# Optimization experiments

Hardware: AMD Instinct MI355X
Metric: run time of the kernel (lower is better)

Reference implementation:

```python
import jax, jax.numpy as jnp
import numpy as np

N_NODES = 50000
N_EDGES = 800000
NODE_DIM = 128
EDGE_DIM = 64
MSG_DIM = 128
IN_DIM = 2 * NODE_DIM + EDGE_DIM  # 320
LN_EPS = 1e-5


def setup_inputs() -> dict:
    key = jax.random.key(0)
    ks = jax.random.split(key, 12)
    nodes = jax.random.normal(ks[0], (N_NODES, NODE_DIM), dtype=jnp.float32)
    edge_index = jax.random.randint(ks[1], (2, N_EDGES), 0, N_NODES, dtype=jnp.int64)
    edges = jax.random.normal(ks[2], (N_EDGES, EDGE_DIM), dtype=jnp.float32)
    # query projection (kaiming-normal weight, zero bias)
    Wq = jax.random.normal(ks[3], (IN_DIM, MSG_DIM), dtype=jnp.float32) * np.sqrt(2.0 / IN_DIM)
    bq = jnp.zeros((MSG_DIM,), dtype=jnp.float32)
    # logit MLP: Linear(IN_DIM->MSG_DIM) -> ReLU -> LayerNorm -> Linear(MSG_DIM->1) -> ReLU
    W1 = jax.random.normal(ks[4], (IN_DIM, MSG_DIM), dtype=jnp.float32) * np.sqrt(1.0 / IN_DIM)
    b1 = jnp.zeros((MSG_DIM,), dtype=jnp.float32)
    gamma = jnp.ones((MSG_DIM,), dtype=jnp.float32)
    beta = jnp.zeros((MSG_DIM,), dtype=jnp.float32)
    W2 = jax.random.normal(ks[5], (MSG_DIM, 1), dtype=jnp.float32) * np.sqrt(1.0 / MSG_DIM)
    b2 = jnp.zeros((1,), dtype=jnp.float32)
    return {"nodes": nodes, "edge_index": edge_index, "edges": edges,
            "Wq": Wq, "bq": bq, "W1": W1, "b1": b1,
            "gamma": gamma, "beta": beta, "W2": W2, "b2": b2}


def _layernorm(h, gamma, beta):
    mu = jnp.mean(h, axis=-1, keepdims=True)
    var = jnp.mean(jnp.square(h - mu), axis=-1, keepdims=True)
    return (h - mu) / jnp.sqrt(var + LN_EPS) * gamma + beta


def _forward(nodes, edges, Wq, bq, W1, b1, gamma, beta, W2, b2, senders, receivers):
    n_nodes = nodes.shape[0]
    x = jnp.concatenate([nodes[senders], nodes[receivers], edges], axis=-1)  # (E, IN_DIM)
    queries = x @ Wq + bq                                                    # (E, MSG_DIM)
    h = jax.nn.relu(x @ W1 + b1)
    h = _layernorm(h, gamma, beta)
    logits = jax.nn.relu(h @ W2 + b2)[:, 0]                                  # (E,)
    # segment softmax over receivers
    seg_max = jax.ops.segment_max(logits, receivers, num_segments=n_nodes)
    seg_max = jnp.where(jnp.isfinite(seg_max), seg_max, 0.0)
    exp_l = jnp.exp(logits - seg_max[receivers])
    seg_sum = jax.ops.segment_sum(exp_l, receivers, num_segments=n_nodes)
    weights = exp_l / (seg_sum[receivers] + 1e-10)                           # (E,)
    messages = queries * weights[:, None]
    out = jax.ops.segment_sum(messages, receivers, num_segments=n_nodes)    # (N, MSG_DIM)
    return jax.nn.leaky_relu(out, negative_slope=0.01)


def reference(nodes, edge_index, edges, Wq, bq, W1, b1, gamma, beta, W2, b2):
    senders, receivers = edge_index[0], edge_index[1]
    return _forward(nodes, edges, Wq, bq, W1, b1, gamma, beta, W2, b2, senders, receivers)
```

## Files before the change

kernel.cpp:

```cpp
#include <hip/hip_runtime.h>
#include <hip/hip_bf16.h>

#define NN 50000
#define NE 800000
#define D 128
#define ED 64
#define IN_DIM 320
#define MB 64
#define KP 328
#define NT (NE / MB)
#define PGRID 512
#define NB ((NN + 255) / 256)

typedef short short8 __attribute__((ext_vector_type(8)));
typedef float f32x4 __attribute__((ext_vector_type(4)));

__device__ __forceinline__ ushort f2b(float f) {
  __hip_bfloat16 h = __float2bfloat16(f);
  return *reinterpret_cast<ushort*>(&h);
}
__device__ __forceinline__ float b2f(ushort u) {
  return __uint_as_float(((uint)u) << 16);
}
__device__ __forceinline__ ushort4 c4(float4 v) {
  ushort4 u; u.x = f2b(v.x); u.y = f2b(v.y); u.z = f2b(v.z); u.w = f2b(v.w);
  return u;
}

__device__ __forceinline__ void gather_regs(
    ushort4 g[20], const int* __restrict__ senders,
    const int* __restrict__ receivers, const float* __restrict__ nodes,
    const float* __restrict__ efeat, int e0, int tid)
{
  const int e = tid >> 2, p = tid & 3;
  const float* ns = nodes + (size_t)senders[e0 + e] * D;
  const float* nr = nodes + (size_t)receivers[e0 + e] * D;
  const float* ef = efeat + (size_t)(e0 + e) * ED;
#pragma unroll
  for (int i = 0; i < 8; ++i) g[i] = c4(*(const float4*)(ns + (p + 4 * i) * 4));
#pragma unroll
  for (int i = 0; i < 8; ++i) g[8 + i] = c4(*(const float4*)(nr + (p + 4 * i) * 4));
#pragma unroll
  for (int i = 0; i < 4; ++i) g[16 + i] = c4(*(const float4*)(ef + (p + 4 * i) * 4));
}

__device__ __forceinline__ void write_xs(
    ushort xs[MB][KP], const ushort4 g[20], int tid)
{
  const int e = tid >> 2, p = tid & 3;
#pragma unroll
  for (int i = 0; i < 8; ++i)
    *reinterpret_cast<ushort4*>(&xs[e][(p + 4 * i) * 4]) = g[i];
#pragma unroll
  for (int i = 0; i < 8; ++i)
    *reinterpret_cast<ushort4*>(&xs[e][128 + (p + 4 * i) * 4]) = g[8 + i];
#pragma unroll
  for (int i = 0; i < 4; ++i)
    *reinterpret_cast<ushort4*>(&xs[e][256 + (p + 4 * i) * 4]) = g[16 + i];
}

__global__ __launch_bounds__(256) void k_wconv(
    const float* __restrict__ Wq, const float* __restrict__ W1,
    ushort* __restrict__ Wqt, ushort* __restrict__ W1t)
{
  int i = blockIdx.x * 256 + threadIdx.x;
  if (i < D * IN_DIM) {
    int n = i / IN_DIM, k = i - n * IN_DIM;
    Wqt[i] = f2b(Wq[k * D + n]);
    W1t[i] = f2b(W1[k * D + n]);
  }
}

__global__ __launch_bounds__(256, 2) void k_fused(
    const float* __restrict__ nodes,
    const int* __restrict__ senders, const int* __restrict__ receivers,
    const float* __restrict__ efeat,
    const ushort* __restrict__ Wqt, const float* __restrict__ bq,
    const ushort* __restrict__ W1t, const float* __restrict__ b1,
    const float* __restrict__ gamma_, const float* __restrict__ beta_,
    const float* __restrict__ W2, const float* __restrict__ b2,
    ushort* __restrict__ queries, float* __restrict__ logits,
    float* __restrict__ seg_max)
{
  __shared__ ushort xs[MB][KP];
  __shared__ float red[MB][4][3];
  const int tid = threadIdx.x;
  const int w = tid >> 6, l = tid & 63, lr = l & 15, lg = l >> 4;
  const int n0 = 32 * w + lr, n1 = 32 * w + 16 + lr;

  const float b1a = b1[n0], b1b = b1[n1];
  const float g0 = gamma_[n0], g1 = gamma_[n1];
  const float be0 = beta_[n0], be1 = beta_[n1];
  const float w20 = W2[n0], w21 = W2[n1];
  const float bq0 = bq[n0], bq1 = bq[n1];
  const float b2s = b2[0];
  const float wg0 = w20 * g0, wg1 = w21 * g1;

  short8 B1r[10][2];
#pragma unroll
  for (int ks = 0; ks < 10; ++ks) {
    B1r[ks][0] = *reinterpret_cast<const short8*>(W1t + n0 * IN_DIM + ks * 32 + lg * 8);
    B1r[ks][1] = *reinterpret_cast<const short8*>(W1t + n1 * IN_DIM + ks * 32 + lg * 8);
  }

  {
    float p1 = wg0 + wg1;
    float p2 = w20 * be0 + w21 * be1;
#pragma unroll
    for (int off = 1; off < 64; off <<= 1) {
      p1 += __shfl_xor(p1, off);
      p2 += __shfl_xor(p2, off);
    }
    if (l == 0) { red[0][w][0] = p1; red[0][w][1] = p2; }
  }
  __syncthreads();
  const float S1  = 0.25f * (red[0][0][0] + red[0][1][0] + red[0][2][0] + red[0][3][0]);
  const float B2t = 0.25f * (red[0][0][1] + red[0][1][1] + red[0][2][1] + red[0][3][1]) + b2s;

  int tile = blockIdx.x;
  ushort4 g[20];
  gather_regs(g, senders, receivers, nodes, efeat, tile * MB, tid);

  while (tile < NT) {
    const int e0 = tile * MB;
    write_xs(xs, g, tid);
    __syncthreads();

    f32x4 aq[4][2] = {};
#pragma unroll 2
    for (int ks = 0; ks < 10; ++ks) {
      short8 Q0 = *reinterpret_cast<const short8*>(Wqt + n0 * IN_DIM + ks * 32 + lg * 8);
      short8 Q1 = *reinterpret_cast<const short8*>(Wqt + n1 * IN_DIM + ks * 32 + lg * 8);
      short8 A[4];
#pragma unroll
      for (int mt = 0; mt < 4; ++mt)
        A[mt] = *reinterpret_cast<const short8*>(&xs[mt * 16 + lr][ks * 32 + lg * 8]);
#pragma unroll
      for (int mt = 0; mt < 4; ++mt) {
        aq[mt][0] = __builtin_amdgcn_mfma_f32_16x16x32_bf16(A[mt], Q0, aq[mt][0], 0, 0, 0);
        aq[mt][1] = __builtin_amdgcn_mfma_f32_16x16x32_bf16(A[mt], Q1, aq[mt][1], 0, 0, 0);
      }
    }
#pragma unroll
    for (int mt = 0; mt < 4; ++mt)
#pragma unroll
      for (int r = 0; r < 4; ++r) {
        int row = mt * 16 + lg * 4 + r;
        queries[(size_t)(e0 + row) * D + n0] = f2b(aq[mt][0][r] + bq0);
        queries[(size_t)(e0 + row) * D + n1] = f2b(aq[mt][1][r] + bq1);
      }

    const int nxt = tile + PGRID;
    if (nxt < NT)
      gather_regs(g, senders, receivers, nodes, efeat, nxt * MB, tid);

    f32x4 ah[4][2] = {};
#pragma unroll
    for (int ks = 0; ks < 10; ++ks) {
      short8 A[4];
#pragma unroll
      for (int mt = 0; mt < 4; ++mt)
        A[mt] = *reinterpret_cast<const short8*>(&xs[mt * 16 + lr][ks * 32 + lg * 8]);
#pragma unroll
      for (int mt = 0; mt < 4; ++mt) {
        ah[mt][0] = __builtin_amdgcn_mfma_f32_16x16x32_bf16(A[mt], B1r[ks][0], ah[mt][0], 0, 0, 0);
        ah[mt][1] = __builtin_amdgcn_mfma_f32_16x16x32_bf16(A[mt], B1r[ks][1], ah[mt][1], 0, 0, 0);
      }
    }

#pragma unroll
    for (int mt = 0; mt < 4; ++mt)
#pragma unroll
      for (int r = 0; r < 4; ++r) {
        float h0 = fmaxf(ah[mt][0][r] + b1a, 0.f);
        float h1 = fmaxf(ah[mt][1][r] + b1b, 0.f);
        float s = h0 + h1;
        float q = h0 * h0 + h1 * h1;
        float t = h0 * wg0 + h1 * wg1;
#pragma unroll
        for (int off = 1; off < 16; off <<= 1) {
          s += __shfl_xor(s, off);
          q += __shfl_xor(q, off);
          t += __shfl_xor(t, off);
        }
        if (lr == mt * 4 + r) {
          int row = mt * 16 + lg * 4 + r;
          red[row][w][0] = s;
          red[row][w][1] = q;
          red[row][w][2] = t;
        }
      }
    __syncthreads();
    if (tid < MB) {
      float s = red[tid][0][0] + red[tid][1][0] + red[tid][2][0] + red[tid][3][0];
      float q = red[tid][0][1] + red[tid][1][1] + red[tid][2][1] + red[tid][3][1];
      float t = red[tid][0][2] + red[tid][1][2] + red[tid][2][2] + red[tid][3][2];
      float mu = s * (1.f / 128.f);
      float var = fmaxf(q * (1.f / 128.f) - mu * mu, 0.f);
      float rs = rsqrtf(var + 1e-5f);
      float logit = fmaxf(rs * (t - mu * S1) + B2t, 0.f);
      logits[e0 + tid] = logit;
      atomicMax((int*)&seg_max[receivers[e0 + tid]], __float_as_int(logit));
    }
    tile = nxt;
  }
}

__global__ __launch_bounds__(256) void k_hist(
    const int* __restrict__ receivers, int* __restrict__ deg)
{
  int e = blockIdx.x * 256 + threadIdx.x;
  if (e < NE) atomicAdd(&deg[receivers[e]], 1);
}

__global__ __launch_bounds__(256) void k_scan1(
    const int* __restrict__ deg, int* __restrict__ bsum)
{
  __shared__ int buf[256];
  int i = blockIdx.x * 256 + threadIdx.x;
  int v = (i < NN) ? deg[i] : 0;
  buf[threadIdx.x] = v;
  __syncthreads();
  for (int off = 128; off > 0; off >>= 1) {
    if (threadIdx.x < off) buf[threadIdx.x] += buf[threadIdx.x + off];
    __syncthreads();
  }
  if (threadIdx.x == 0) bsum[blockIdx.x] = buf[0];
}

__global__ __launch_bounds__(256) void k_scan2(
    const int* __restrict__ bsum, int* __restrict__ bpre, int* __restrict__ offs)
{
  __shared__ int buf[256];
  int t = threadIdx.x;
  int v = (t < NB) ? bsum[t] : 0;
  buf[t] = v;
  __syncthreads();
  for (int off = 1; off < 256; off <<= 1) {
    int x = (t >= off) ? buf[t - off] : 0;
    __syncthreads();
    buf[t] += x;
    __syncthreads();
  }
  if (t < NB) bpre[t] = buf[t] - v;
  if (t == 0) offs[NN] = NE;
}

__global__ __launch_bounds__(256) void k_scan3(
    const int* __restrict__ deg, const int* __restrict__ bpre,
    int* __restrict__ offs, int* __restrict__ cursor)
{
  __shared__ int buf[256];
  int t = threadIdx.x;
  int i = blockIdx.x * 256 + t;
  int v = (i < NN) ? deg[i] : 0;
  buf[t] = v;
  __syncthreads();
  for (int off = 1; off < 256; off <<= 1) {
    int x = (t >= off) ? buf[t - off] : 0;
    __syncthreads();
    buf[t] += x;
    __syncthreads();
  }
  if (i < NN) {
    int o = bpre[blockIdx.x] + buf[t] - v;
    offs[i] = o;
    cursor[i] = o;
  }
}

__global__ __launch_bounds__(256) void k_bucket(
    const int* __restrict__ receivers, int* __restrict__ cursor,
    int* __restrict__ ebuf)
{
  int e = blockIdx.x * 256 + threadIdx.x;
  if (e < NE) {
    int pos = atomicAdd(&cursor[receivers[e]], 1);
    ebuf[pos] = e;
  }
}

__global__ __launch_bounds__(256) void k_bsort(
    const int* __restrict__ offs, int* __restrict__ ebuf)
{
  int node = blockIdx.x * 256 + threadIdx.x;
  if (node >= NN) return;
  const int beg = offs[node], end = offs[node + 1];
  for (int i = beg + 1; i < end; ++i) {
    int v = ebuf[i];
    int j = i - 1;
    while (j >= beg && ebuf[j] > v) { ebuf[j + 1] = ebuf[j]; --j; }
    ebuf[j + 1] = v;
  }
}

__global__ __launch_bounds__(256) void k_out(
    const int* __restrict__ offs, const int* __restrict__ ebuf,
    const float* __restrict__ logits, const float* __restrict__ seg_max,
    const ushort* __restrict__ queries, float* __restrict__ out)
{
  int node = blockIdx.x * 4 + (threadIdx.x >> 6);
  if (node >= NN) return;
  const int l = threadIdx.x & 63;
  const int beg = offs[node], end = offs[node + 1];
  const float smax = seg_max[node];
  float a0 = 0.f, a1 = 0.f, den = 0.f;
  for (int i = beg; i < end; ++i) {
    int e = ebuf[i];
    float ex = expf(logits[e] - smax);
    ushort2 q = *reinterpret_cast<const ushort2*>(queries + (size_t)e * D + 2 * l);
    a0 = fmaf(ex, b2f(q.x), a0);
    a1 = fmaf(ex, b2f(q.y), a1);
    den += ex;
  }
  float inv = 1.f / (den + 1e-10f);
  float v0 = a0 * inv, v1 = a1 * inv;
  v0 = v0 > 0.f ? v0 : 0.01f * v0;
  v1 = v1 > 0.f ? v1 : 0.01f * v1;
  *reinterpret_cast<float2*>(out + (size_t)node * D + 2 * l) = make_float2(v0, v1);
}

extern "C" void kernel_launch(void* const* d_in, const int* in_sizes, int n_in,
                              void* d_out, int out_size, void* d_ws, size_t ws_size,
                              hipStream_t stream) {
  const float* nodes  = (const float*)d_in[0];
  const int*   eidx   = (const int*)d_in[1];
  const float* efeat  = (const float*)d_in[2];
  const float* Wq     = (const float*)d_in[3];
  const float* bq     = (const float*)d_in[4];
  const float* W1     = (const float*)d_in[5];
  const float* b1     = (const float*)d_in[6];
  const float* gamma_ = (const float*)d_in[7];
  const float* beta_  = (const float*)d_in[8];
  const float* W2     = (const float*)d_in[9];
  const float* b2     = (const float*)d_in[10];
  const int* senders   = eidx;
  const int* receivers = eidx + NE;

  float* ws       = (float*)d_ws;
  float* logits   = ws;
  float* seg_max  = ws + NE;
  int*   deg      = (int*)(seg_max + NN);
  int*   offs     = deg + NN;
  int*   cursor   = offs + NN + 1;
  int*   bsum     = cursor + NN;
  int*   bpre     = bsum + 256;
  int*   ebuf     = bpre + 256 + 3;
  ushort* Wqt     = (ushort*)(ebuf + NE);
  ushort* W1t     = Wqt + D * IN_DIM;
  ushort* queries = W1t + D * IN_DIM;

  hipMemsetAsync(seg_max, 0, NN * sizeof(float), stream);
  hipMemsetAsync(deg, 0, NN * sizeof(int), stream);

  k_wconv<<<(D * IN_DIM + 255) / 256, 256, 0, stream>>>(Wq, W1, Wqt, W1t);

  k_hist<<<(NE + 255) / 256, 256, 0, stream>>>(receivers, deg);
  k_scan1<<<NB, 256, 0, stream>>>(deg, bsum);
  k_scan2<<<1, 256, 0, stream>>>(bsum, bpre, offs);
  k_scan3<<<NB, 256, 0, stream>>>(deg, bpre, offs, cursor);
  k_bucket<<<(NE + 255) / 256, 256, 0, stream>>>(receivers, cursor, ebuf);
  k_bsort<<<NB, 256, 0, stream>>>(offs, ebuf);

  k_fused<<<PGRID, 256, 0, stream>>>(nodes, senders, receivers, efeat,
                                     Wqt, bq, W1t, b1, gamma_, beta_, W2, b2,
                                     queries, logits, seg_max);

  k_out<<<(NN + 3) / 4, 256, 0, stream>>>(offs, ebuf, logits, seg_max,
                                          queries, (float*)d_out);
}
```

Measured before the change: 595.8 us.

## Scatter queries and logits into receiver-sorted order and merge the GEMM loops

Builds an inverse permutation (edge to its sorted position) and has the fused kernel write queries and logits directly at their receiver-sorted positions. The output kernel can then read them contiguously instead of going through the ebuf indirection. The two MFMA loops are merged into a single pass over the shared tile, and W1 is loaded from global memory each iteration instead of being held in registers, which lowers register pressure. The cost is scattered row writes in the fused kernel plus one extra small permutation kernel.

```diff
diff --git a/kernel.cpp b/kernel.cpp
--- a/kernel.cpp
+++ b/kernel.cpp
@@ -79,11 +79,13 @@
     const ushort* __restrict__ W1t, const float* __restrict__ b1,
     const float* __restrict__ gamma_, const float* __restrict__ beta_,
     const float* __restrict__ W2, const float* __restrict__ b2,
-    ushort* __restrict__ queries, float* __restrict__ logits,
+    const int* __restrict__ pos,
+    ushort* __restrict__ queries, float* __restrict__ lgp,
     float* __restrict__ seg_max)
 {
   __shared__ ushort xs[MB][KP];
   __shared__ float red[MB][4][3];
+  __shared__ int pos_s[MB];
   const int tid = threadIdx.x;
   const int w = tid >> 6, l = tid & 63, lr = l & 15, lg = l >> 4;
   const int n0 = 32 * w + lr, n1 = 32 * w + 16 + lr;
@@ -96,13 +98,6 @@
   const float b2s = b2[0];
   const float wg0 = w20 * g0, wg1 = w21 * g1;
 
-  short8 B1r[10][2];
-#pragma unroll
-  for (int ks = 0; ks < 10; ++ks) {
-    B1r[ks][0] = *reinterpret_cast<const short8*>(W1t + n0 * IN_DIM + ks * 32 + lg * 8);
-    B1r[ks][1] = *reinterpret_cast<const short8*>(W1t + n1 * IN_DIM + ks * 32 + lg * 8);
-  }
-
   {
     float p1 = wg0 + wg1;
     float p2 = w20 * be0 + w21 * be1;
@@ -123,14 +118,18 @@
 
   while (tile < NT) {
     const int e0 = tile * MB;
+    if (tid < MB) pos_s[tid] = pos[e0 + tid];
     write_xs(xs, g, tid);
     __syncthreads();
 
     f32x4 aq[4][2] = {};
+    f32x4 ah[4][2] = {};
 #pragma unroll 2
     for (int ks = 0; ks < 10; ++ks) {
       short8 Q0 = *reinterpret_cast<const short8*>(Wqt + n0 * IN_DIM + ks * 32 + lg * 8);
       short8 Q1 = *reinterpret_cast<const short8*>(Wqt + n1 * IN_DIM + ks * 32 + lg * 8);
+      short8 Y0 = *reinterpret_cast<const short8*>(W1t + n0 * IN_DIM + ks * 32 + lg * 8);
+      short8 Y1 = *reinterpret_cast<const short8*>(W1t + n1 * IN_DIM + ks * 32 + lg * 8);
       short8 A[4];
 #pragma unroll
       for (int mt = 0; mt < 4; ++mt)
@@ -139,34 +138,24 @@
       for (int mt = 0; mt < 4; ++mt) {
         aq[mt][0] = __builtin_amdgcn_mfma_f32_16x16x32_bf16(A[mt], Q0, aq[mt][0], 0, 0, 0);
         aq[mt][1] = __builtin_amdgcn_mfma_f32_16x16x32_bf16(A[mt], Q1, aq[mt][1], 0, 0, 0);
+        ah[mt][0] = __builtin_amdgcn_mfma_f32_16x16x32_bf16(A[mt], Y0, ah[mt][0], 0, 0, 0);
+        ah[mt][1] = __builtin_amdgcn_mfma_f32_16x16x32_bf16(A[mt], Y1, ah[mt][1], 0, 0, 0);
       }
     }
+
 #pragma unroll
     for (int mt = 0; mt < 4; ++mt)
 #pragma unroll
       for (int r = 0; r < 4; ++r) {
         int row = mt * 16 + lg * 4 + r;
-        queries[(size_t)(e0 + row) * D + n0] = f2b(aq[mt][0][r] + bq0);
-        queries[(size_t)(e0 + row) * D + n1] = f2b(aq[mt][1][r] + bq1);
+        int p = pos_s[row];
+        queries[(size_t)p * D + n0] = f2b(aq[mt][0][r] + bq0);
+        queries[(size_t)p * D + n1] = f2b(aq[mt][1][r] + bq1);
       }
 
     const int nxt = tile + PGRID;
     if (nxt < NT)
       gather_regs(g, senders, receivers, nodes, efeat, nxt * MB, tid);
-
-    f32x4 ah[4][2] = {};
-#pragma unroll
-    for (int ks = 0; ks < 10; ++ks) {
-      short8 A[4];
-#pragma unroll
-      for (int mt = 0; mt < 4; ++mt)
-        A[mt] = *reinterpret_cast<const short8*>(&xs[mt * 16 + lr][ks * 32 + lg * 8]);
-#pragma unroll
-      for (int mt = 0; mt < 4; ++mt) {
-        ah[mt][0] = __builtin_amdgcn_mfma_f32_16x16x32_bf16(A[mt], B1r[ks][0], ah[mt][0], 0, 0, 0);
-        ah[mt][1] = __builtin_amdgcn_mfma_f32_16x16x32_bf16(A[mt], B1r[ks][1], ah[mt][1], 0, 0, 0);
-      }
-    }
 
 #pragma unroll
     for (int mt = 0; mt < 4; ++mt)
@@ -199,7 +188,7 @@
       float var = fmaxf(q * (1.f / 128.f) - mu * mu, 0.f);
       float rs = rsqrtf(var + 1e-5f);
       float logit = fmaxf(rs * (t - mu * S1) + B2t, 0.f);
-      logits[e0 + tid] = logit;
+      lgp[pos[e0 + tid]] = logit;
       atomicMax((int*)&seg_max[receivers[e0 + tid]], __float_as_int(logit));
     }
     tile = nxt;
@@ -294,10 +283,17 @@
   }
 }
 
+__global__ __launch_bounds__(256) void k_pos(
+    const int* __restrict__ ebuf, int* __restrict__ pos)
+{
+  int i = blockIdx.x * 256 + threadIdx.x;
+  if (i < NE) pos[ebuf[i]] = i;
+}
+
 __global__ __launch_bounds__(256) void k_out(
-    const int* __restrict__ offs, const int* __restrict__ ebuf,
-    const float* __restrict__ logits, const float* __restrict__ seg_max,
-    const ushort* __restrict__ queries, float* __restrict__ out)
+    const int* __restrict__ offs, const float* __restrict__ lgp,
+    const float* __restrict__ seg_max, const ushort* __restrict__ queries,
+    float* __restrict__ out)
 {
   int node = blockIdx.x * 4 + (threadIdx.x >> 6);
   if (node >= NN) return;
@@ -306,9 +302,8 @@
   const float smax = seg_max[node];
   float a0 = 0.f, a1 = 0.f, den = 0.f;
   for (int i = beg; i < end; ++i) {
-    int e = ebuf[i];
-    float ex = expf(logits[e] - smax);
-    ushort2 q = *reinterpret_cast<const ushort2*>(queries + (size_t)e * D + 2 * l);
+    float ex = expf(lgp[i] - smax);
+    ushort2 q = *reinterpret_cast<const ushort2*>(queries + (size_t)i * D + 2 * l);
     a0 = fmaf(ex, b2f(q.x), a0);
     a1 = fmaf(ex, b2f(q.y), a1);
     den += ex;
@@ -338,7 +333,7 @@
   const int* receivers = eidx + NE;
 
   float* ws       = (float*)d_ws;
-  float* logits   = ws;
+  float* lgp      = ws;
   float* seg_max  = ws + NE;
   int*   deg      = (int*)(seg_max + NN);
   int*   offs     = deg + NN;
@@ -346,7 +341,8 @@
   int*   bsum     = cursor + NN;
   int*   bpre     = bsum + 256;
   int*   ebuf     = bpre + 256 + 3;
-  ushort* Wqt     = (ushort*)(ebuf + NE);
+  int*   pos      = ebuf + NE;
+  ushort* Wqt     = (ushort*)(pos + NE);
   ushort* W1t     = Wqt + D * IN_DIM;
   ushort* queries = W1t + D * IN_DIM;
 
@@ -361,11 +357,12 @@
   k_scan3<<<NB, 256, 0, stream>>>(deg, bpre, offs, cursor);
   k_bucket<<<(NE + 255) / 256, 256, 0, stream>>>(receivers, cursor, ebuf);
   k_bsort<<<NB, 256, 0, stream>>>(offs, ebuf);
+  k_pos<<<(NE + 255) / 256, 256, 0, stream>>>(ebuf, pos);
 
   k_fused<<<PGRID, 256, 0, stream>>>(nodes, senders, receivers, efeat,
                                      Wqt, bq, W1t, b1, gamma_, beta_, W2, b2,
-                                     queries, logits, seg_max);
-
-  k_out<<<(NN + 3) / 4, 256, 0, stream>>>(offs, ebuf, logits, seg_max,
+                                     pos, queries, lgp, seg_max);
+
+  k_out<<<(NN + 3) / 4, 256, 0, stream>>>(offs, lgp, seg_max,
                                           queries, (float*)d_out);
 }
```

Result: slower. 634.7 us (+6.5%).
